# Performance work log

Measured on AMD Instinct MI355X. Metric: run time of the kernel, lower is better.

## Reference

```python
import jax, jax.numpy as jnp
import numpy as np

THETA = 10000.0
D_K = 64
NUM_HEADS = 16


def _rope_tables(token_positions):
    # token_positions: [s] int -> cos/sin: [s, d_k//2]
    pos = token_positions.astype(jnp.float32)
    dim_idx = jnp.arange(0, D_K, 2, dtype=jnp.float32)
    freqs = 1.0 / (THETA ** (dim_idx / D_K))  # [d_k//2]
    ang = pos[:, None] * freqs[None, :]       # [s, d_k//2]
    return jnp.cos(ang), jnp.sin(ang)


def _apply_rope(x, cos, sin):
    # x: [b, h, s, d_k]; cos/sin: [s, d_k//2] broadcast over b, h
    x1 = x[..., 0::2]
    x2 = x[..., 1::2]
    r1 = x1 * cos - x2 * sin
    r2 = x2 * cos + x1 * sin
    return jnp.stack([r1, r2], axis=-1).reshape(x.shape)


def setup_inputs() -> dict:
    key = jax.random.key(0)
    ks = jax.random.split(key, 5)
    b, s, d = 2, 2048, 1024
    x = jax.random.normal(ks[0], (b, s, d), dtype=jnp.float32)
    token_positions = jnp.arange(s, dtype=jnp.int32)
    scale = (2.0 / (d + d)) ** 0.5
    Wq = jax.random.normal(ks[1], (d, d), dtype=jnp.float32) * scale
    Wk = jax.random.normal(ks[2], (d, d), dtype=jnp.float32) * scale
    Wv = jax.random.normal(ks[3], (d, d), dtype=jnp.float32) * scale
    Wo = jax.random.normal(ks[4], (d, d), dtype=jnp.float32) * scale
    return {"x": x, "token_positions": token_positions,
            "Wq": Wq, "Wk": Wk, "Wv": Wv, "Wo": Wo}


def reference(x, token_positions, Wq, Wk, Wv, Wo):
    b, s, d_model = x.shape
    h, d_k = NUM_HEADS, D_K

    def split_heads(t):
        return t.reshape(b, s, h, d_k).transpose(0, 2, 1, 3)  # [b, h, s, d_k]

    Q = split_heads(jnp.einsum('ij,bsj->bsi', Wq, x))
    K = split_heads(jnp.einsum('ij,bsj->bsi', Wk, x))
    V = split_heads(jnp.einsum('ij,bsj->bsi', Wv, x))

    cos, sin = _rope_tables(token_positions)
    Q = _apply_rope(Q, cos, sin)
    K = _apply_rope(K, cos, sin)

    scale = 1.0 / jnp.sqrt(jnp.float32(d_k))
    scores = jnp.einsum('bhqd,bhkd->bhqk', Q, K) * scale  # [b, h, s, s]
    causal = jnp.tril(jnp.ones((s, s), dtype=bool))
    scores = jnp.where(causal, scores, -jnp.inf)
    attn = jax.nn.softmax(scores, axis=-1)
    out = jnp.einsum('bhqk,bhkd->bhqd', attn, V)
    out = out.transpose(0, 2, 1, 3).reshape(b, s, d_model)
    return jnp.einsum('ij,bsj->bsi', Wo, out)
```

## Files before the change

kernel.cpp:

```cpp
#include <hip/hip_runtime.h>
#include <hip/hip_bf16.h>


typedef __attribute__((ext_vector_type(8))) __bf16 bf16x8;
typedef __attribute__((ext_vector_type(4))) float f32x4;
typedef __attribute__((ext_vector_type(16))) float f32x16;
typedef __attribute__((ext_vector_type(4))) int int4v;
typedef __attribute__((ext_vector_type(2))) unsigned int uint2v;

#define MFMA16(a, b, c) __builtin_amdgcn_mfma_f32_16x16x32_bf16(a, b, c, 0, 0, 0)
#define MFMA32(a, b, c) __builtin_amdgcn_mfma_f32_32x32x16_bf16(a, b, c, 0, 0, 0)

__device__ inline unsigned short f2b(float f) {
  unsigned u = __builtin_bit_cast(unsigned, f);
  u = (u + 0x7FFF + ((u >> 16) & 1)) >> 16;
  return (unsigned short)u;
}

__device__ inline float b2f(unsigned short u) {
  return __builtin_bit_cast(float, ((unsigned)u) << 16);
}

__device__ inline unsigned pk2b(float lo, float hi) {
  return (unsigned)f2b(lo) | ((unsigned)f2b(hi) << 16);
}

__device__ inline unsigned cvtpk(float lo, float hi) {
  unsigned r;
  asm("v_cvt_pk_bf16_f32 %0, %1, %2" : "=v"(r) : "v"(lo), "v"(hi));
  return r;
}

__device__ inline void plswap(unsigned a, unsigned b, unsigned& o0, unsigned& o1) {
#if __has_builtin(__builtin_amdgcn_permlane32_swap)
  auto r = __builtin_amdgcn_permlane32_swap(a, b, false, false);
  o0 = r[0];
  o1 = r[1];
#else
  unsigned sa = (unsigned)__shfl_xor((int)a, 32, 64);
  unsigned sb = (unsigned)__shfl_xor((int)b, 32, 64);
  bool hi = (threadIdx.x & 32) != 0;
  o0 = hi ? sb : a;
  o1 = hi ? b : sa;
#endif
}

__device__ inline float fexp2(float x) {
#if __has_builtin(__builtin_amdgcn_exp2f)
  return __builtin_amdgcn_exp2f(x);
#else
  return exp2f(x);
#endif
}


__device__ inline void cvt8(const float* __restrict__ s, unsigned short* __restrict__ d,
                            int i, float sc) {
  float4 v0 = *(const float4*)(s + i);
  float4 v1 = *(const float4*)(s + i + 4);
  int4v p;
  p[0] = (int)pk2b(v0.x * sc, v0.y * sc);
  p[1] = (int)pk2b(v0.z * sc, v0.w * sc);
  p[2] = (int)pk2b(v1.x * sc, v1.y * sc);
  p[3] = (int)pk2b(v1.z * sc, v1.w * sc);
  *(int4v*)(d + i) = p;
}

__global__ __launch_bounds__(256) void prep_kernel(
    const float* __restrict__ x, const float* __restrict__ Wq,
    const float* __restrict__ Wk, const float* __restrict__ Wv,
    const float* __restrict__ Wo, const int* __restrict__ tp,
    unsigned short* __restrict__ xb, unsigned short* __restrict__ Wqkvb,
    unsigned short* __restrict__ Wob, float* __restrict__ cosT,
    float* __restrict__ sinT) {
  int t = blockIdx.x * 256 + threadIdx.x;
  if (t < 524288) {
    cvt8(x, xb, t * 8, 1.0f);
  } else if (t < 655360) {
    cvt8(Wq, Wqkvb, (t - 524288) * 8, 0.18033688f);
  } else if (t < 786432) {
    cvt8(Wk, Wqkvb + 1048576, (t - 655360) * 8, 1.0f);
  } else if (t < 917504) {
    cvt8(Wv, Wqkvb + 2097152, (t - 786432) * 8, 1.0f);
  } else if (t < 1048576) {
    cvt8(Wo, Wob, (t - 917504) * 8, 1.0f);
  } else {
    int base = (t - 1048576) * 8;
#pragma unroll
    for (int j = 0; j < 8; ++j) {
      int idx = base + j;
      int p = idx >> 5, i = idx & 31;
      float pos = (float)tp[p];
      float freq = powf(10000.0f, -(float)i / 32.0f);
      float ang = pos * freq;
      cosT[idx] = cosf(ang);
      sinT[idx] = sinf(ang);
    }
  }
}


__device__ __forceinline__ void g_stage_qkv(const unsigned short* __restrict__ A,
                                            const unsigned short* __restrict__ B,
                                            unsigned short* __restrict__ As,
                                            unsigned short* __restrict__ Bs,
                                            int m0, int n0, int k0, int w, int lane) {
  const int srow = lane >> 3;
  const int schunk = (lane & 7) ^ srow;
#pragma unroll
  for (int c = 0; c < 4; ++c) {
    const int rb = w * 32 + c * 8;
    const unsigned short* ga = A + (size_t)(m0 + rb + srow) * 1024 + k0 + schunk * 8;
    __builtin_amdgcn_global_load_lds(
        (const __attribute__((address_space(1))) void*)ga,
        (__attribute__((address_space(3))) void*)(As + rb * 64), 16, 0, 0);
  }
#pragma unroll
  for (int c = 0; c < 3; ++c) {
    const int rb = w * 24 + c * 8;
    const int rl = rb + srow;
    const int rB = n0 + (rl & 224) + ((rl & 15) << 1) + ((rl >> 4) & 1);
    const unsigned short* gb = B + (size_t)rB * 1024 + k0 + schunk * 8;
    __builtin_amdgcn_global_load_lds(
        (const __attribute__((address_space(1))) void*)gb,
        (__attribute__((address_space(3))) void*)(Bs + rb * 64), 16, 0, 0);
  }
}


__global__ __launch_bounds__(512, 2) void gemm_qkv_kernel(
    const unsigned short* __restrict__ A,
    const unsigned short* __restrict__ B,
    unsigned short* __restrict__ Qb, unsigned short* __restrict__ Kb,
    unsigned short* __restrict__ VbT,
    const float* __restrict__ cosT, const float* __restrict__ sinT) {
  __shared__ unsigned short As[2][256 * 64];
  __shared__ unsigned short Bs[2][192 * 64];
  const int bid = blockIdx.x;
  const int xcd = bid & 7, q = bid >> 3;
  const int mg = xcd >> 1, ng = xcd & 1;
  const int m0 = (mg * 4 + (q & 3)) * 256;
  const int n0 = (ng * 8 + (q >> 2)) * 192;
  const int tid = threadIdx.x, w = tid >> 6, lane = tid & 63;
  const int l15 = lane & 15, l4 = lane >> 4;
  const int wr = w & 3, wc = w >> 2;

  f32x4 acc[4][6] = {};

  g_stage_qkv(A, B, As[0], Bs[0], m0, n0, 0, w, lane);

  int cur = 0;
  for (int k0 = 0; k0 < 1024; k0 += 64) {
    __builtin_amdgcn_s_barrier();
    if (k0 + 64 < 1024) {
      g_stage_qkv(A, B, As[cur ^ 1], Bs[cur ^ 1], m0, n0, k0 + 64, w, lane);
      asm volatile("s_waitcnt vmcnt(7)" ::: "memory");
    } else {
      asm volatile("s_waitcnt vmcnt(0)" ::: "memory");
    }
    __builtin_amdgcn_sched_barrier(0);

    const unsigned short* as = As[cur];
    const unsigned short* bs = Bs[cur];
#pragma unroll
    for (int kk = 0; kk < 2; ++kk) {
      bf16x8 af[4], bfr[6];
#pragma unroll
      for (int m = 0; m < 4; m++) {
        const int row = wr * 64 + m * 16 + l15;
        af[m] = *(const bf16x8*)(&as[row * 64 + (((kk * 4 + l4) ^ (l15 & 7)) * 8)]);
      }
#pragma unroll
      for (int n = 0; n < 6; n++) {
        const int row = wc * 96 + n * 16 + l15;
        bfr[n] = *(const bf16x8*)(&bs[row * 64 + (((kk * 4 + l4) ^ (l15 & 7)) * 8)]);
      }
#pragma unroll
      for (int m = 0; m < 4; m++)
#pragma unroll
        for (int n = 0; n < 6; n++)
          acc[m][n] = MFMA16(af[m], bfr[n], acc[m][n]);
    }
    cur ^= 1;
  }

#pragma unroll
  for (int k = 0; k < 3; k++) {
    const int gcol = n0 + wc * 96 + k * 32 + 2 * l15;
    const int region = gcol >> 10;
    if (region < 2) {
      unsigned short* dst = (region == 0) ? Qb : Kb;
      const int col = gcol & 1023;
      const int pi = (gcol & 63) >> 1;
#pragma unroll
      for (int m = 0; m < 4; m++) {
        const int row0 = m0 + wr * 64 + m * 16 + l4 * 4;
#pragma unroll
        for (int r = 0; r < 4; r++) {
          const int pos = (row0 + r) & 2047;
          float c = cosT[pos * 32 + pi], s = sinT[pos * 32 + pi];
          float v0 = acc[m][2 * k][r], v1 = acc[m][2 * k + 1][r];
          float r1 = fmaf(v0, c, -v1 * s);
          float r2 = fmaf(v1, c, v0 * s);
          *(unsigned*)(dst + (size_t)(row0 + r) * 1024 + col) = pk2b(r1, r2);
        }
      }
    } else {
      const int dkg = gcol - 2048;
      const int h = dkg >> 6, dk = dkg & 63;
#pragma unroll
      for (int m = 0; m < 4; m++) {
        const int row0 = m0 + wr * 64 + m * 16 + l4 * 4;
        const int bb = row0 >> 11, seq = row0 & 2047;
        unsigned short* vp = VbT + (size_t)(bb * 16 + h) * 131072 + dk * 2048 + seq;
        uint2v e = {pk2b(acc[m][2 * k][0], acc[m][2 * k][1]),
                    pk2b(acc[m][2 * k][2], acc[m][2 * k][3])};
        *(uint2v*)vp = e;
        uint2v o = {pk2b(acc[m][2 * k + 1][0], acc[m][2 * k + 1][1]),
                    pk2b(acc[m][2 * k + 1][2], acc[m][2 * k + 1][3])};
        *(uint2v*)(vp + 2048) = o;
      }
    }
  }
}


__device__ __forceinline__ void g_stage_out(const unsigned short* __restrict__ A,
                                            const unsigned short* __restrict__ B,
                                            unsigned short* __restrict__ As,
                                            unsigned short* __restrict__ Bs,
                                            int m0, int n0, int k0, int w, int lane) {
  const int srow = lane >> 3;
  const int schunk = (lane & 7) ^ srow;
#pragma unroll
  for (int c = 0; c < 2; ++c) {
    const int rb = w * 16 + c * 8;
    const unsigned short* ga = A + (size_t)(m0 + rb + srow) * 1024 + k0 + schunk * 8;
    __builtin_amdgcn_global_load_lds(
        (const __attribute__((address_space(1))) void*)ga,
        (__attribute__((address_space(3))) void*)(As + rb * 64), 16, 0, 0);
    const int rl = rb + srow;
    const int rB = n0 + (rl & 96) + ((rl & 15) << 1) + ((rl >> 4) & 1);
    const unsigned short* gb = B + (size_t)rB * 1024 + k0 + schunk * 8;
    __builtin_amdgcn_global_load_lds(
        (const __attribute__((address_space(1))) void*)gb,
        (__attribute__((address_space(3))) void*)(Bs + rb * 64), 16, 0, 0);
  }
}


__global__ __launch_bounds__(512, 2) void gemm_out_kernel(
    const unsigned short* __restrict__ A,
    const unsigned short* __restrict__ B,
    float* __restrict__ out) {
  __shared__ unsigned short As[2][128 * 64];
  __shared__ unsigned short Bs[2][128 * 64];
  const int bid = blockIdx.x;
  const int sw = (bid & 7) * 32 + (bid >> 3);
  const int n0 = (sw % 8) * 128, m0 = (sw / 8) * 128;
  const int tid = threadIdx.x, w = tid >> 6, lane = tid & 63;
  const int l15 = lane & 15, l4 = lane >> 4;
  const int wr = w >> 2, wc = w & 3;

  f32x4 acc[4][2] = {};

  g_stage_out(A, B, As[0], Bs[0], m0, n0, 0, w, lane);

  int cur = 0;
  for (int k0 = 0; k0 < 1024; k0 += 64) {
    __builtin_amdgcn_s_barrier();
    if (k0 + 64 < 1024) {
      g_stage_out(A, B, As[cur ^ 1], Bs[cur ^ 1], m0, n0, k0 + 64, w, lane);
      asm volatile("s_waitcnt vmcnt(4)" ::: "memory");
    } else {
      asm volatile("s_waitcnt vmcnt(0)" ::: "memory");
    }
    __builtin_amdgcn_sched_barrier(0);

    const unsigned short* as = As[cur];
    const unsigned short* bs = Bs[cur];
#pragma unroll
    for (int kk = 0; kk < 2; ++kk) {
      bf16x8 af[4], bfr[2];
#pragma unroll
      for (int m = 0; m < 4; m++) {
        const int row = wr * 64 + m * 16 + l15;
        af[m] = *(const bf16x8*)(&as[row * 64 + (((kk * 4 + l4) ^ (l15 & 7)) * 8)]);
      }
#pragma unroll
      for (int n = 0; n < 2; n++) {
        const int row = wc * 32 + n * 16 + l15;
        bfr[n] = *(const bf16x8*)(&bs[row * 64 + (((kk * 4 + l4) ^ (l15 & 7)) * 8)]);
      }
#pragma unroll
      for (int m = 0; m < 4; m++)
#pragma unroll
        for (int n = 0; n < 2; n++)
          acc[m][n] = MFMA16(af[m], bfr[n], acc[m][n]);
    }
    cur ^= 1;
  }

#pragma unroll
  for (int m = 0; m < 4; m++) {
    const int row0 = m0 + wr * 64 + m * 16 + l4 * 4;
    const int col = n0 + wc * 32 + 2 * l15;
#pragma unroll
    for (int r = 0; r < 4; r++) {
      float2 v = {acc[m][0][r], acc[m][1][r]};
      *(float2*)(out + (size_t)(row0 + r) * 1024 + col) = v;
    }
  }
}


__device__ __forceinline__ void stage_tiles(const unsigned short* __restrict__ Kgb,
                                            const unsigned short* __restrict__ Vgb,
                                            unsigned short* KsBuf, unsigned short* VsBuf,
                                            int kv0, int w, int lane) {
#pragma unroll
  for (int c = 0; c < 2; ++c) {
    const int rowbase = w * 16 + c * 8;
    const int row = rowbase + (lane >> 3);
    const int chunk = (lane & 7) ^ (lane >> 3);
    const unsigned short* gk = Kgb + (size_t)(kv0 + row) * 1024 + chunk * 8;
    __builtin_amdgcn_global_load_lds(
        (const __attribute__((address_space(1))) void*)gk,
        (__attribute__((address_space(3))) void*)(KsBuf + rowbase * 64), 16, 0, 0);
    const unsigned short* gv = Vgb + (size_t)row * 2048 + kv0 + chunk * 8;
    __builtin_amdgcn_global_load_lds(
        (const __attribute__((address_space(1))) void*)gv,
        (__attribute__((address_space(3))) void*)(VsBuf + rowbase * 64), 16, 0, 0);
  }
}

__device__ __forceinline__ void attn_stream(
    int qt, int t0, int t1, bool finalize,
    int b, int h, int w, int lane,
    const unsigned short* __restrict__ Qb,
    const unsigned short* __restrict__ Kgb,
    const unsigned short* __restrict__ Vgb,
    unsigned short* __restrict__ outBase, int ostride,
    float* __restrict__ statsOut,
    unsigned short (*Ks)[64 * 64], unsigned short (*Vs)[64 * 64]) {
  const int l31 = lane & 31, l32 = lane >> 5;
  const int sw = l31 & 7;

  const unsigned short* qptr =
      Qb + (size_t)(b * 2048 + qt * 128 + w * 32 + l31) * 1024 + h * 64 + l32 * 8;
  bf16x8 qa[4];
#pragma unroll
  for (int kk = 0; kk < 4; ++kk) qa[kk] = *(const bf16x8*)(qptr + kk * 16);

  f32x16 oacc[2] = {};
  float m = -3e38f, l = 0.f;

  stage_tiles(Kgb, Vgb, Ks[0], Vs[0], t0 * 64, w, lane);
  if (t0 + 1 < t1) stage_tiles(Kgb, Vgb, Ks[1], Vs[1], (t0 + 1) * 64, w, lane);

  for (int t = t0; t < t1; ++t) {
    const int it = t - t0;
    if ((it & 1) == 0) __builtin_amdgcn_s_barrier();
    if (t + 2 < t1)
      stage_tiles(Kgb, Vgb, Ks[(it + 2) & 3], Vs[(it + 2) & 3], (t + 2) * 64, w, lane);
    if (t + 2 < t1) {
      asm volatile("s_waitcnt vmcnt(8)" ::: "memory");
    } else if (t + 1 < t1) {
      asm volatile("s_waitcnt vmcnt(4)" ::: "memory");
    } else {
      asm volatile("s_waitcnt vmcnt(0)" ::: "memory");
    }
    __builtin_amdgcn_sched_barrier(0);

    const char* ksb = (const char*)Ks[it & 3];
    f32x16 st[2];
    __builtin_amdgcn_s_setprio(1);
#pragma unroll
    for (int f = 0; f < 2; ++f) {
      const char* kb = ksb + (f * 32 + l31) * 128;
      f32x16 z = {};
#pragma unroll
      for (int kk = 0; kk < 4; ++kk) {
        bf16x8 kf = *(const bf16x8*)(kb + ((((kk << 1) | l32) ^ sw) * 16));
        z = MFMA32(kf, qa[kk], z);
      }
      st[f] = z;
    }
    __builtin_amdgcn_s_setprio(0);

    if (t >= 2 * qt + (w >> 1)) {
      const int qg = qt * 128 + w * 32 + l31;
      const int kvb = t * 64 + 4 * l32;
#pragma unroll
      for (int f = 0; f < 2; ++f)
#pragma unroll
        for (int reg = 0; reg < 16; ++reg) {
          int kv = kvb + 32 * f + (reg & 3) + 8 * (reg >> 2);
          if (kv > qg) st[f][reg] = -3e38f;
        }
    }

    float a8[8];
#pragma unroll
    for (int j = 0; j < 8; ++j)
      a8[j] = fmaxf(fmaxf(st[0][j], st[0][j + 8]), fmaxf(st[1][j], st[1][j + 8]));
    float pm = fmaxf(fmaxf(fmaxf(a8[0], a8[1]), fmaxf(a8[2], a8[3])),
                     fmaxf(fmaxf(a8[4], a8[5]), fmaxf(a8[6], a8[7])));
    pm = fmaxf(pm, __shfl_xor(pm, 32, 64));

    if (!__all(pm - m <= 8.0f)) {
      float mn = fmaxf(m, pm);
      float al = fexp2(m - mn);
      l *= al;
#pragma unroll
      for (int df = 0; df < 2; ++df)
#pragma unroll
        for (int reg = 0; reg < 16; ++reg) oacc[df][reg] *= al;
      m = mn;
    }

    unsigned pku[2][4][2];
    float rs0 = 0.f, rs1 = 0.f;
#pragma unroll
    for (int f = 0; f < 2; ++f)
#pragma unroll
      for (int rr = 0; rr < 4; ++rr)
#pragma unroll
        for (int i = 0; i < 2; ++i) {
          float p0 = fexp2(st[f][4 * rr + 2 * i] - m);
          float p1 = fexp2(st[f][4 * rr + 2 * i + 1] - m);
          rs0 += p0; rs1 += p1;
          pku[f][rr][i] = cvtpk(p0, p1);
        }
    float rs = rs0 + rs1;
    rs += __shfl_xor(rs, 32, 64);
    l += rs;

    union FB { unsigned u[4]; bf16x8 v; };
    FB pfrag[4];
#pragma unroll
    for (int kk = 0; kk < 4; ++kk) {
      const int f = kk >> 1, kl = kk & 1;
      unsigned o00, o10, o01, o11;
      plswap(pku[f][2 * kl][0], pku[f][2 * kl + 1][0], o00, o10);
      plswap(pku[f][2 * kl][1], pku[f][2 * kl + 1][1], o01, o11);
      pfrag[kk].u[0] = o00; pfrag[kk].u[1] = o01;
      pfrag[kk].u[2] = o10; pfrag[kk].u[3] = o11;
    }

    const char* vsb = (const char*)Vs[it & 3];
    __builtin_amdgcn_s_setprio(1);
#pragma unroll
    for (int df = 0; df < 2; ++df) {
      const char* vb = vsb + (df * 32 + l31) * 128;
#pragma unroll
      for (int kk = 0; kk < 4; ++kk) {
        bf16x8 vf = *(const bf16x8*)(vb + ((((kk << 1) | l32) ^ sw) * 16));
        oacc[df] = MFMA32(vf, pfrag[kk].v, oacc[df]);
      }
    }
    __builtin_amdgcn_s_setprio(0);
  }

  const float sc = finalize ? (1.0f / l) : 1.0f;
  unsigned short* ob = outBase + (size_t)(w * 32 + l31) * ostride + 4 * l32;
#pragma unroll
  for (int df = 0; df < 2; ++df)
#pragma unroll
    for (int rr = 0; rr < 4; ++rr)
#pragma unroll
      for (int i = 0; i < 2; ++i) {
        *(unsigned*)(ob + df * 32 + rr * 8 + 2 * i) =
            pk2b(oacc[df][4 * rr + 2 * i] * sc, oacc[df][4 * rr + 2 * i + 1] * sc);
      }
  if (!finalize && l32 == 0) {
    float2 st2 = {m, l};
    *(float2*)(statsOut + (w * 32 + l31) * 2) = st2;
  }
}

__global__ __launch_bounds__(256, 2) void attn_kernel(
    const unsigned short* __restrict__ Qb,
    const unsigned short* __restrict__ Kb,
    const unsigned short* __restrict__ VbT,
    unsigned short* __restrict__ Ob,
    unsigned short* __restrict__ P2,
    float* __restrict__ stats1, float* __restrict__ stats2) {
  __shared__ unsigned short Ks[4][64 * 64];
  __shared__ unsigned short Vs[4][64 * 64];
  const int bh = blockIdx.x;
  const int y = blockIdx.y;
  const int j = y >> 1, half = y & 1;
  const int b = bh >> 4, h = bh & 15;
  const int qtB = 15 - j;
  const int x = 15 - 2 * j;
  const int cid = bh * 8 + j;
  const int tid = threadIdx.x, w = tid >> 6, lane = tid & 63;

  const unsigned short* Kgb = Kb + (size_t)b * 2048 * 1024 + h * 64;
  const unsigned short* Vgb = VbT + (size_t)bh * 131072;

  if (half == 0) {
    attn_stream(qtB, 0, x, false, b, h, w, lane, Qb, Kgb, Vgb,
                Ob + (size_t)(b * 2048 + qtB * 128) * 1024 + h * 64, 1024,
                stats1 + cid * 256, Ks, Vs);
    __syncthreads();
    attn_stream(j, 0, 2 * j + 2, true, b, h, w, lane, Qb, Kgb, Vgb,
                Ob + (size_t)(b * 2048 + j * 128) * 1024 + h * 64, 1024,
                nullptr, Ks, Vs);
  } else {
    attn_stream(qtB, x, 32 - 2 * j, false, b, h, w, lane, Qb, Kgb, Vgb,
                P2 + (size_t)cid * 8192, 64,
                stats2 + cid * 256, Ks, Vs);
  }
}


__global__ __launch_bounds__(256) void merge_kernel(
    unsigned short* __restrict__ Ob, const unsigned short* __restrict__ P2,
    const float* __restrict__ stats1, const float* __restrict__ stats2) {
  const int cid = blockIdx.x;
  const int bh = cid >> 3, j = cid & 7, qt = 15 - j;
  const int b = bh >> 4, h = bh & 15;
  const int tid = threadIdx.x;
  const int r = tid >> 1, ch = (tid & 1) * 32;

  const float m1 = stats1[cid * 256 + r * 2], l1 = stats1[cid * 256 + r * 2 + 1];
  const float m2 = stats2[cid * 256 + r * 2], l2 = stats2[cid * 256 + r * 2 + 1];
  const float M = fmaxf(m1, m2);
  const float a1 = fexp2(m1 - M), a2 = fexp2(m2 - M);
  const float invL = 1.0f / (l1 * a1 + l2 * a2);
  const float c1 = a1 * invL, c2 = a2 * invL;

  unsigned short* o1 = Ob + (size_t)(b * 2048 + qt * 128 + r) * 1024 + h * 64 + ch;
  const unsigned short* o2 = P2 + (size_t)cid * 8192 + r * 64 + ch;
#pragma unroll
  for (int i = 0; i < 32; i += 8) {
    int4v v1 = *(const int4v*)(o1 + i);
    int4v v2 = *(const int4v*)(o2 + i);
    int4v ro;
#pragma unroll
    for (int k = 0; k < 4; ++k) {
      unsigned u1 = (unsigned)v1[k], u2 = (unsigned)v2[k];
      float lo = b2f((unsigned short)u1) * c1 + b2f((unsigned short)u2) * c2;
      float hi = b2f((unsigned short)(u1 >> 16)) * c1 + b2f((unsigned short)(u2 >> 16)) * c2;
      ro[k] = (int)pk2b(lo, hi);
    }
    *(int4v*)(o1 + i) = ro;
  }
}


extern "C" void kernel_launch(void* const* d_in, const int* in_sizes, int n_in,
                              void* d_out, int out_size, void* d_ws, size_t ws_size,
                              hipStream_t stream) {
  (void)in_sizes; (void)n_in; (void)out_size; (void)ws_size;
  const float* x  = (const float*)d_in[0];
  const int*  tp  = (const int*)d_in[1];
  const float* Wq = (const float*)d_in[2];
  const float* Wk = (const float*)d_in[3];
  const float* Wv = (const float*)d_in[4];
  const float* Wo = (const float*)d_in[5];
  float* out = (float*)d_out;

  char* ws = (char*)d_ws;
  unsigned short* xb    = (unsigned short*)(ws);
  unsigned short* Ob    = (unsigned short*)(ws);
  unsigned short* Wqkvb = (unsigned short*)(ws + (8ull << 20));
  unsigned short* P2    = (unsigned short*)(ws + (8ull << 20));
  unsigned short* Wob   = (unsigned short*)(ws + (14ull << 20));
  unsigned short* Qb    = (unsigned short*)(ws + (16ull << 20));
  unsigned short* Kb    = (unsigned short*)(ws + (24ull << 20));
  unsigned short* VbT   = (unsigned short*)(ws + (32ull << 20));
  float* cosT   = (float*)(ws + (40ull << 20));
  float* sinT   = (float*)(ws + (40ull << 20) + 262144);
  float* stats1 = (float*)(ws + (40ull << 20));
  float* stats2 = (float*)(ws + (40ull << 20) + 262144);

  prep_kernel<<<4128, 256, 0, stream>>>(x, Wq, Wk, Wv, Wo, tp, xb, Wqkvb, Wob, cosT, sinT);
  gemm_qkv_kernel<<<256, 512, 0, stream>>>(xb, Wqkvb, Qb, Kb, VbT, cosT, sinT);
  attn_kernel<<<dim3(32, 16), 256, 0, stream>>>(Qb, Kb, VbT, Ob, P2, stats1, stats2);
  merge_kernel<<<256, 256, 0, stream>>>(Ob, P2, stats1, stats2);
  gemm_out_kernel<<<256, 512, 0, stream>>>(Ob, Wob, out);
}
```

Measured before the change: 103.7 us.

## Double attention query tile to 256 rows with 8 waves per block

Raises the attention block from 4 to 8 waves so each block handles a 256-row query tile, which halves the grid and lets each staged K/V tile be shared by twice as many query rows. Each wave now stages one 8-row slice per tile instead of two, and the vmcnt waits shrink to match. The split of causal work between the two halves and the merge kernel are rescaled to the new tile size. The cost is fewer, larger blocks: there are 256 blocks instead of 512, which can leave the machine less evenly loaded, and the register limit per thread is tighter at 512 threads.

```diff
diff --git a/kernel.cpp b/kernel.cpp
--- a/kernel.cpp
+++ b/kernel.cpp
@@ -318,20 +318,17 @@
                                             const unsigned short* __restrict__ Vgb,
                                             unsigned short* KsBuf, unsigned short* VsBuf,
                                             int kv0, int w, int lane) {
-#pragma unroll
-  for (int c = 0; c < 2; ++c) {
-    const int rowbase = w * 16 + c * 8;
-    const int row = rowbase + (lane >> 3);
-    const int chunk = (lane & 7) ^ (lane >> 3);
-    const unsigned short* gk = Kgb + (size_t)(kv0 + row) * 1024 + chunk * 8;
-    __builtin_amdgcn_global_load_lds(
-        (const __attribute__((address_space(1))) void*)gk,
-        (__attribute__((address_space(3))) void*)(KsBuf + rowbase * 64), 16, 0, 0);
-    const unsigned short* gv = Vgb + (size_t)row * 2048 + kv0 + chunk * 8;
-    __builtin_amdgcn_global_load_lds(
-        (const __attribute__((address_space(1))) void*)gv,
-        (__attribute__((address_space(3))) void*)(VsBuf + rowbase * 64), 16, 0, 0);
-  }
+  const int rowbase = w * 8;
+  const int row = rowbase + (lane >> 3);
+  const int chunk = (lane & 7) ^ (lane >> 3);
+  const unsigned short* gk = Kgb + (size_t)(kv0 + row) * 1024 + chunk * 8;
+  __builtin_amdgcn_global_load_lds(
+      (const __attribute__((address_space(1))) void*)gk,
+      (__attribute__((address_space(3))) void*)(KsBuf + rowbase * 64), 16, 0, 0);
+  const unsigned short* gv = Vgb + (size_t)row * 2048 + kv0 + chunk * 8;
+  __builtin_amdgcn_global_load_lds(
+      (const __attribute__((address_space(1))) void*)gv,
+      (__attribute__((address_space(3))) void*)(VsBuf + rowbase * 64), 16, 0, 0);
 }
 
 __device__ __forceinline__ void attn_stream(
@@ -347,7 +344,7 @@
   const int sw = l31 & 7;
 
   const unsigned short* qptr =
-      Qb + (size_t)(b * 2048 + qt * 128 + w * 32 + l31) * 1024 + h * 64 + l32 * 8;
+      Qb + (size_t)(b * 2048 + qt * 256 + w * 32 + l31) * 1024 + h * 64 + l32 * 8;
   bf16x8 qa[4];
 #pragma unroll
   for (int kk = 0; kk < 4; ++kk) qa[kk] = *(const bf16x8*)(qptr + kk * 16);
@@ -364,9 +361,9 @@
     if (t + 2 < t1)
       stage_tiles(Kgb, Vgb, Ks[(it + 2) & 3], Vs[(it + 2) & 3], (t + 2) * 64, w, lane);
     if (t + 2 < t1) {
-      asm volatile("s_waitcnt vmcnt(8)" ::: "memory");
+      asm volatile("s_waitcnt vmcnt(4)" ::: "memory");
     } else if (t + 1 < t1) {
-      asm volatile("s_waitcnt vmcnt(4)" ::: "memory");
+      asm volatile("s_waitcnt vmcnt(2)" ::: "memory");
     } else {
       asm volatile("s_waitcnt vmcnt(0)" ::: "memory");
     }
@@ -388,8 +385,8 @@
     }
     __builtin_amdgcn_s_setprio(0);
 
-    if (t >= 2 * qt + (w >> 1)) {
-      const int qg = qt * 128 + w * 32 + l31;
+    if (t >= 4 * qt + (w >> 1)) {
+      const int qg = qt * 256 + w * 32 + l31;
       const int kvb = t * 64 + 4 * l32;
 #pragma unroll
       for (int f = 0; f < 2; ++f)
@@ -479,7 +476,7 @@
   }
 }
 
-__global__ __launch_bounds__(256, 2) void attn_kernel(
+__global__ __launch_bounds__(512, 2) void attn_kernel(
     const unsigned short* __restrict__ Qb,
     const unsigned short* __restrict__ Kb,
     const unsigned short* __restrict__ VbT,
@@ -490,11 +487,11 @@
   __shared__ unsigned short Vs[4][64 * 64];
   const int bh = blockIdx.x;
   const int y = blockIdx.y;
-  const int j = y >> 1, half = y & 1;
+  const int i = y >> 1, half = y & 1;
   const int b = bh >> 4, h = bh & 15;
-  const int qtB = 15 - j;
-  const int x = 15 - 2 * j;
-  const int cid = bh * 8 + j;
+  const int qtB = 7 - i;
+  const int x = 14 - 4 * i;
+  const int cid = bh * 4 + i;
   const int tid = threadIdx.x, w = tid >> 6, lane = tid & 63;
 
   const unsigned short* Kgb = Kb + (size_t)b * 2048 * 1024 + h * 64;
@@ -502,16 +499,16 @@
 
   if (half == 0) {
     attn_stream(qtB, 0, x, false, b, h, w, lane, Qb, Kgb, Vgb,
-                Ob + (size_t)(b * 2048 + qtB * 128) * 1024 + h * 64, 1024,
-                stats1 + cid * 256, Ks, Vs);
+                Ob + (size_t)(b * 2048 + qtB * 256) * 1024 + h * 64, 1024,
+                stats1 + cid * 512, Ks, Vs);
     __syncthreads();
-    attn_stream(j, 0, 2 * j + 2, true, b, h, w, lane, Qb, Kgb, Vgb,
-                Ob + (size_t)(b * 2048 + j * 128) * 1024 + h * 64, 1024,
+    attn_stream(i, 0, 4 * i + 4, true, b, h, w, lane, Qb, Kgb, Vgb,
+                Ob + (size_t)(b * 2048 + i * 256) * 1024 + h * 64, 1024,
                 nullptr, Ks, Vs);
   } else {
-    attn_stream(qtB, x, 32 - 2 * j, false, b, h, w, lane, Qb, Kgb, Vgb,
-                P2 + (size_t)cid * 8192, 64,
-                stats2 + cid * 256, Ks, Vs);
+    attn_stream(qtB, x, 32 - 4 * i, false, b, h, w, lane, Qb, Kgb, Vgb,
+                P2 + (size_t)cid * 16384, 64,
+                stats2 + cid * 512, Ks, Vs);
   }
 }
 
@@ -520,24 +517,23 @@
     unsigned short* __restrict__ Ob, const unsigned short* __restrict__ P2,
     const float* __restrict__ stats1, const float* __restrict__ stats2) {
   const int cid = blockIdx.x;
-  const int bh = cid >> 3, j = cid & 7, qt = 15 - j;
+  const int bh = cid >> 2, i = cid & 3, qt = 7 - i;
   const int b = bh >> 4, h = bh & 15;
-  const int tid = threadIdx.x;
-  const int r = tid >> 1, ch = (tid & 1) * 32;
-
-  const float m1 = stats1[cid * 256 + r * 2], l1 = stats1[cid * 256 + r * 2 + 1];
-  const float m2 = stats2[cid * 256 + r * 2], l2 = stats2[cid * 256 + r * 2 + 1];
+  const int r = threadIdx.x;
+
+  const float m1 = stats1[cid * 512 + r * 2], l1 = stats1[cid * 512 + r * 2 + 1];
+  const float m2 = stats2[cid * 512 + r * 2], l2 = stats2[cid * 512 + r * 2 + 1];
   const float M = fmaxf(m1, m2);
   const float a1 = fexp2(m1 - M), a2 = fexp2(m2 - M);
   const float invL = 1.0f / (l1 * a1 + l2 * a2);
   const float c1 = a1 * invL, c2 = a2 * invL;
 
-  unsigned short* o1 = Ob + (size_t)(b * 2048 + qt * 128 + r) * 1024 + h * 64 + ch;
-  const unsigned short* o2 = P2 + (size_t)cid * 8192 + r * 64 + ch;
-#pragma unroll
-  for (int i = 0; i < 32; i += 8) {
-    int4v v1 = *(const int4v*)(o1 + i);
-    int4v v2 = *(const int4v*)(o2 + i);
+  unsigned short* o1 = Ob + (size_t)(b * 2048 + qt * 256 + r) * 1024 + h * 64;
+  const unsigned short* o2 = P2 + (size_t)cid * 16384 + r * 64;
+#pragma unroll
+  for (int i2 = 0; i2 < 64; i2 += 8) {
+    int4v v1 = *(const int4v*)(o1 + i2);
+    int4v v2 = *(const int4v*)(o2 + i2);
     int4v ro;
 #pragma unroll
     for (int k = 0; k < 4; ++k) {
@@ -546,7 +542,7 @@
       float hi = b2f((unsigned short)(u1 >> 16)) * c1 + b2f((unsigned short)(u2 >> 16)) * c2;
       ro[k] = (int)pk2b(lo, hi);
     }
-    *(int4v*)(o1 + i) = ro;
+    *(int4v*)(o1 + i2) = ro;
   }
 }
 
@@ -579,7 +575,7 @@
 
   prep_kernel<<<4128, 256, 0, stream>>>(x, Wq, Wk, Wv, Wo, tp, xb, Wqkvb, Wob, cosT, sinT);
   gemm_qkv_kernel<<<256, 512, 0, stream>>>(xb, Wqkvb, Qb, Kb, VbT, cosT, sinT);
-  attn_kernel<<<dim3(32, 16), 256, 0, stream>>>(Qb, Kb, VbT, Ob, P2, stats1, stats2);
-  merge_kernel<<<256, 256, 0, stream>>>(Ob, P2, stats1, stats2);
+  attn_kernel<<<dim3(32, 8), 512, 0, stream>>>(Qb, Kb, VbT, Ob, P2, stats1, stats2);
+  merge_kernel<<<128, 256, 0, stream>>>(Ob, P2, stats1, stats2);
   gemm_out_kernel<<<256, 512, 0, stream>>>(Ob, Wob, out);
 }
```

Measured after the change: 108.0 us. 4.1% more time.
